# Kernel optimization log

Hardware: AMD Instinct MI355X
Metric: run time of the kernel (lower is better)

The kernel has to match this reference:

```python
import jax, jax.numpy as jnp
import numpy as np

EMBED = 1280
H = 20
D = 64
MAX_CACHE_LEN = 2048
NEG = -1e30


def setup_inputs() -> dict:
    key = jax.random.key(0)
    ks = jax.random.split(key, 6)
    w = lambda k: jax.random.normal(k, (EMBED, EMBED), dtype=jnp.float32) * 0.02
    return {
        "hidden_states": jax.random.normal(ks[0], (1, 2048, EMBED), dtype=jnp.float32),
        "wq": w(ks[1]), "bq": jnp.zeros((EMBED,), jnp.float32),
        "wk": w(ks[2]),
        "wv": w(ks[3]), "bv": jnp.zeros((EMBED,), jnp.float32),
        "wo": w(ks[4]), "bo": jnp.zeros((EMBED,), jnp.float32),
        "pos_int": 0,
    }


def reference(hidden_states, wq, bq, wk, wv, bv, wo, bo, pos_int):
    B, T, E = hidden_states.shape
    scale = D ** -0.5
    # projections (torch Linear: x @ W^T + b); Whisper k_proj has no bias
    q = (hidden_states @ wq.T + bq).reshape(B, T, H, D).transpose(0, 2, 1, 3)
    k = (hidden_states @ wk.T).reshape(B, T, H, D).transpose(0, 2, 1, 3)
    v = (hidden_states @ wv.T + bv).reshape(B, T, H, D).transpose(0, 2, 1, 3)
    # static KV-cache update (ETKVCache.update): write k,v at [pos:pos+T]
    k_cache = jnp.zeros((B, H, MAX_CACHE_LEN, D), hidden_states.dtype)
    v_cache = jnp.zeros((B, H, MAX_CACHE_LEN, D), hidden_states.dtype)
    k_cache = jax.lax.dynamic_update_slice(k_cache, k, (0, 0, pos_int, 0))
    v_cache = jax.lax.dynamic_update_slice(v_cache, v, (0, 0, pos_int, 0))
    end_pos = pos_int + T
    k_win = k_cache[:, :, :end_pos, :]  # [B,H,S,D]
    v_win = v_cache[:, :, :end_pos, :]
    # SDPA with is_causal=True: torch uses top-left aligned tril(T, S) mask
    scores = jnp.einsum("bhtd,bhsd->bhts", q, k_win) * scale
    mask = jnp.tril(jnp.ones((T, end_pos), dtype=bool))
    scores = jnp.where(mask, scores, NEG)
    attn = jax.nn.softmax(scores, axis=-1)
    out = jnp.einsum("bhts,bhsd->bhtd", attn, v_win)
    out = out.transpose(0, 2, 1, 3).reshape(B, T, H * D)
    return out @ wo.T + bo
```

## Files before the change

kernel.cpp:

```cpp
#include <hip/hip_runtime.h>
#include <hip/hip_bf16.h>

typedef __bf16 bf16;
typedef __bf16 bf16x8 __attribute__((ext_vector_type(8)));
typedef float  f32x4  __attribute__((ext_vector_type(4)));
typedef float  f32x16 __attribute__((ext_vector_type(16)));
typedef unsigned int u32;
typedef u32 u32x4 __attribute__((ext_vector_type(4)));

#define AS1 __attribute__((address_space(1)))
#define AS3 __attribute__((address_space(3)))

#define T_LEN 2048
#define EMB   1280
#define NH    20
#define HD    64

#define NCHUNK_PER_HEAD 40

#define QSCALE 0.18033688011112042f

__device__ __forceinline__ void gl_lds16(const void* gsrc, void* ldst) {
  __builtin_amdgcn_global_load_lds((AS1 void*)const_cast<void*>(gsrc),
                                   (AS3 void*)ldst, 16, 0, 0);
}

__global__ __launch_bounds__(256) void cvt_all(
    const float* __restrict__ hs, const float* __restrict__ wq,
    const float* __restrict__ wk, const float* __restrict__ wv,
    const float* __restrict__ wo, bf16* __restrict__ out) {
  const int HS8 = T_LEN * EMB / 8;
  const int W8  = EMB * EMB / 8;
  int i = blockIdx.x * 256 + threadIdx.x;
  const float* src;
  bf16* dst;
  int off;
  if (i < HS8)              { src = hs; dst = out;                              off = i; }
  else if (i < HS8 + W8)    { src = wq; dst = out + (size_t)T_LEN * EMB;        off = i - HS8; }
  else if (i < HS8 + 2*W8)  { src = wk; dst = out + (size_t)T_LEN*EMB +   (size_t)EMB*EMB; off = i - HS8 - W8; }
  else if (i < HS8 + 3*W8)  { src = wv; dst = out + (size_t)T_LEN*EMB + 2*(size_t)EMB*EMB; off = i - HS8 - 2*W8; }
  else if (i < HS8 + 4*W8)  { src = wo; dst = out + (size_t)T_LEN*EMB + 3*(size_t)EMB*EMB; off = i - HS8 - 3*W8; }
  else return;
  const float4* p4 = (const float4*)src;
  float4 a = p4[2 * off], b = p4[2 * off + 1];
  bf16x8 o;
  o[0] = (bf16)a.x; o[1] = (bf16)a.y; o[2] = (bf16)a.z; o[3] = (bf16)a.w;
  o[4] = (bf16)b.x; o[5] = (bf16)b.y; o[6] = (bf16)b.z; o[7] = (bf16)b.w;
  *(bf16x8*)(dst + (size_t)off * 8) = o;
}

template<int MT>
__global__ __launch_bounds__(256, 2) void gemm_nt(
    const bf16* __restrict__ hsb, const bf16* __restrict__ aob,
    const bf16* __restrict__ wqb, const bf16* __restrict__ wkb,
    const bf16* __restrict__ wvb, const bf16* __restrict__ wob,
    const float* __restrict__ bq, const float* __restrict__ bv,
    const float* __restrict__ bo,
    bf16* __restrict__ Qb, bf16* __restrict__ Kb, bf16* __restrict__ VTb,
    float* __restrict__ Out, int kind)
{
  constexpr int BM = MT * 32;
  constexpr int NK = EMB / 64;
  __shared__ alignas(16) bf16 As[2][BM * 64];
  __shared__ alignas(16) bf16 Bs[2][128 * 64];

  const int mode = (kind == 0) ? (int)blockIdx.y : 3;
  const bf16* A = (kind == 0) ? hsb : aob;
  const bf16* B = (mode == 0) ? wqb : (mode == 1) ? wkb : (mode == 2) ? wvb : wob;

  const int bm = blockIdx.x / 10;
  const int bn = blockIdx.x % 10;
  const int lane = threadIdx.x & 63;
  const int w = threadIdx.x >> 6;
  const int wr = w >> 1, wc = w & 1;
  const int g = lane >> 4, c = lane & 15;

  const f32x4 z4 = {0.f, 0.f, 0.f, 0.f};
  f32x4 acc[MT][4];
  #pragma unroll
  for (int i = 0; i < MT; ++i)
    #pragma unroll
    for (int j = 0; j < 4; ++j) acc[i][j] = z4;

  auto STAGE = [&](int b, int kt) {
    #pragma unroll
    for (int i = 0; i < MT; ++i) {
      const int call = w * MT + i;
      const int slot = call * 1024 + lane * 16;
      const int row = slot >> 7;
      const int scb = (slot & 127) ^ ((row & 7) << 4);
      gl_lds16((const char*)A + (size_t)(bm * BM + row) * (EMB * 2) + kt * 128 + scb,
               (char*)As[b] + call * 1024);
    }
    #pragma unroll
    for (int i = 0; i < 4; ++i) {
      const int call = w * 4 + i;
      const int slot = call * 1024 + lane * 16;
      const int row = slot >> 7;
      const int scb = (slot & 127) ^ ((row & 7) << 4);
      gl_lds16((const char*)B + (size_t)(bn * 128 + row) * (EMB * 2) + kt * 128 + scb,
               (char*)Bs[b] + call * 1024);
    }
  };

  STAGE(0, 0);
  for (int kt = 0; kt < NK; ++kt) {
    const int cur = kt & 1;
    STAGE(cur ^ 1, kt + 1 < NK ? kt + 1 : kt);
    if constexpr (MT == 4) asm volatile("s_waitcnt vmcnt(8)" ::: "memory");
    else                   asm volatile("s_waitcnt vmcnt(6)" ::: "memory");
    __builtin_amdgcn_s_barrier();
    asm volatile("" ::: "memory");
    const bf16* Asc = As[cur];
    const bf16* Bsc = Bs[cur];
    #pragma unroll
    for (int kc = 0; kc < 2; ++kc) {
      bf16x8 af[MT], bfr[4];
      #pragma unroll
      for (int mt = 0; mt < MT; ++mt) {
        const int row = wr * (MT * 16) + mt * 16 + c;
        const int off = row * 128 + ((kc * 64 + g * 16) ^ ((row & 7) << 4));
        af[mt] = *(const bf16x8*)((const char*)Asc + off);
      }
      #pragma unroll
      for (int nt = 0; nt < 4; ++nt) {
        const int row = wc * 64 + nt * 16 + c;
        const int off = row * 128 + ((kc * 64 + g * 16) ^ ((row & 7) << 4));
        bfr[nt] = *(const bf16x8*)((const char*)Bsc + off);
      }
      #pragma unroll
      for (int mt = 0; mt < MT; ++mt)
        #pragma unroll
        for (int nt = 0; nt < 4; ++nt)
          acc[mt][nt] = __builtin_amdgcn_mfma_f32_16x16x32_bf16(af[mt], bfr[nt],
                                                                acc[mt][nt], 0, 0, 0);
    }
    asm volatile("" ::: "memory");
    __builtin_amdgcn_s_barrier();
  }

  #pragma unroll
  for (int mt = 0; mt < MT; ++mt) {
    const int t0 = bm * BM + wr * (MT * 16) + mt * 16 + g * 4;
    #pragma unroll
    for (int nt = 0; nt < 4; ++nt) {
      const int n = bn * 128 + wc * 64 + nt * 16 + c;
      const int h = n >> 6, d = n & 63;
      #pragma unroll
      for (int r = 0; r < 4; ++r) {
        const int t = t0 + r;
        float v = acc[mt][nt][r];
        if (mode == 0) {
          v = (v + bq[n]) * QSCALE;
          Qb[((size_t)h * T_LEN + t) * HD + d] = (bf16)v;
        } else if (mode == 1) {
          Kb[((size_t)h * T_LEN + t) * HD + d] = (bf16)v;
        } else if (mode == 2) {
          v += bv[n];
          VTb[((size_t)h * HD + d) * T_LEN + t] = (bf16)v;
        } else {
          Out[(size_t)t * EMB + n] = v + bo[n];
        }
      }
    }
  }
}

__global__ __launch_bounds__(256, 4) void attn_fwd(
    const bf16* __restrict__ Qb, const bf16* __restrict__ Kb,
    const bf16* __restrict__ VTb, bf16* __restrict__ AOb,
    bf16* __restrict__ Pob, float* __restrict__ Pml)
{
  __shared__ alignas(16) bf16 kbuf[2][64 * 64];
  __shared__ alignas(16) bf16 vbuf[2][64 * 64];

  const int bid = blockIdx.x;
  const int h   = bid / NCHUNK_PER_HEAD;
  const int idx = (NCHUNK_PER_HEAD - 1) - bid % NCHUNK_PER_HEAD;
  int qb, ch, nch;
  if (idx < 4)       { qb = idx;                ch = 0;      nch = 1; }
  else if (idx < 12) { int t = idx - 4;  qb = 4 + (t >> 1);  ch = t & 1;  nch = 2; }
  else if (idx < 24) { int t = idx - 12; qb = 8 + t / 3;     ch = t % 3;  nch = 3; }
  else               { int t = idx - 24; qb = 12 + (t >> 2); ch = t & 3;  nch = 4; }
  const int nj = 2 * qb + 2;
  const int j0 = ch * 8;
  const int j1 = (j0 + 8 < nj) ? j0 + 8 : nj;

  const int lane = threadIdx.x & 63;
  const int w  = threadIdx.x >> 6;
  const int l31 = lane & 31;
  const int hi  = lane >> 5;
  const int q0 = qb * 128;
  const int q  = q0 + w * 32 + l31;

  bf16x8 qf[4];
  {
    const char* qrow = (const char*)Qb + ((size_t)h * T_LEN + q) * (HD * 2);
    #pragma unroll
    for (int ds = 0; ds < 4; ++ds)
      qf[ds] = *(const bf16x8*)(qrow + ds * 32 + hi * 16);
  }

  f32x16 oacc[2];
  #pragma unroll
  for (int r = 0; r < 16; ++r) { oacc[0][r] = 0.f; oacc[1][r] = 0.f; }
  float m_r = -1e30f, ls = 0.f;

  auto STAGE = [&](int b, int j) {
    const int s0 = j * 64;
    #pragma unroll
    for (int i = 0; i < 2; ++i) {
      const int call = w * 2 + i;
      const int slot = call * 1024 + lane * 16;
      const int row = slot >> 7;
      const int col = (slot & 127) ^ ((row & 7) << 4);
      gl_lds16((const char*)Kb + ((size_t)h * T_LEN + s0 + row) * (HD * 2) + col,
               (char*)kbuf[b] + call * 1024);
      gl_lds16((const char*)VTb + (((size_t)h * HD + row) * T_LEN + s0) * 2 + col,
               (char*)vbuf[b] + call * 1024);
    }
  };

  auto AFRAG = [&](const bf16* buf, int rblk, int colb) -> bf16x8 {
    const int row = rblk * 32 + l31;
    const int off = row * 128 + ((colb + hi * 16) ^ ((row & 7) << 4));
    return *(const bf16x8*)((const char*)buf + off);
  };

  STAGE(0, j0);
  int cur = 0;
  for (int j = j0; j < j1; ++j) {
    STAGE(cur ^ 1, j + 1 < j1 ? j + 1 : j);
    asm volatile("s_waitcnt vmcnt(4)" ::: "memory");
    __builtin_amdgcn_s_barrier();
    asm volatile("" ::: "memory");

    f32x16 sv[2];
    #pragma unroll
    for (int r = 0; r < 16; ++r) { sv[0][r] = 0.f; sv[1][r] = 0.f; }
    #pragma unroll
    for (int ds = 0; ds < 4; ++ds) {
      #pragma unroll
      for (int sb = 0; sb < 2; ++sb) {
        bf16x8 kf = AFRAG(kbuf[cur], sb, ds * 32);
        sv[sb] = __builtin_amdgcn_mfma_f32_32x32x16_bf16(kf, qf[ds], sv[sb], 0, 0, 0);
      }
    }

    if (j >= 2 * qb) {
      const int s0 = j * 64;
      #pragma unroll
      for (int sb = 0; sb < 2; ++sb)
        #pragma unroll
        for (int r = 0; r < 16; ++r) {
          const int s = s0 + sb * 32 + (r & 3) + 8 * (r >> 2) + 4 * hi;
          if (s > q) sv[sb][r] = -1e30f;
        }
    }

    float pm = sv[0][0];
    #pragma unroll
    for (int r = 1; r < 16; ++r) pm = fmaxf(pm, sv[0][r]);
    #pragma unroll
    for (int r = 0; r < 16; ++r) pm = fmaxf(pm, sv[1][r]);
    pm = fmaxf(pm, __shfl_xor(pm, 32));
    const float mn = fmaxf(m_r, pm);
    const float sc = __builtin_amdgcn_exp2f(m_r - mn);
    m_r = mn;
    float ps = 0.f;
    #pragma unroll
    for (int sb = 0; sb < 2; ++sb)
      #pragma unroll
      for (int r = 0; r < 16; ++r) {
        const float p = __builtin_amdgcn_exp2f(sv[sb][r] - mn);
        sv[sb][r] = p;
        ps += p;
      }
    ls = ls * sc + ps;
    oacc[0] *= sc;
    oacc[1] *= sc;

    u32 wds[16], xds[16];
    #pragma unroll
    for (int i = 0; i < 8; ++i) {
      asm("v_cvt_pk_bf16_f32 %0, %1, %2" : "=v"(wds[i])     : "v"(sv[0][2*i]), "v"(sv[0][2*i+1]));
      asm("v_cvt_pk_bf16_f32 %0, %1, %2" : "=v"(wds[8 + i]) : "v"(sv[1][2*i]), "v"(sv[1][2*i+1]));
    }
    #pragma unroll
    for (int i = 0; i < 16; ++i) xds[i] = (u32)__shfl_xor((int)wds[i], 32);

    #pragma unroll
    for (int ks = 0; ks < 4; ++ks) {
      const int o = (ks >> 1) * 8 + (ks & 1) * 4;
      u32x4 fw;
      fw.x = hi ? xds[o + 2] : wds[o];
      fw.y = hi ? xds[o + 3] : wds[o + 1];
      fw.z = hi ? wds[o + 2] : xds[o];
      fw.w = hi ? wds[o + 3] : xds[o + 1];
      bf16x8 pf = __builtin_bit_cast(bf16x8, fw);
      #pragma unroll
      for (int db = 0; db < 2; ++db) {
        bf16x8 vf = AFRAG(vbuf[cur], db, ks * 32);
        oacc[db] = __builtin_amdgcn_mfma_f32_32x32x16_bf16(vf, pf, oacc[db], 0, 0, 0);
      }
    }

    asm volatile("" ::: "memory");
    __builtin_amdgcn_s_barrier();
    cur ^= 1;
  }

  const float lt = ls + __shfl_xor(ls, 32);

  if (nch == 1) {
    const float inv = 1.f / lt;
    char* orow = (char*)AOb + ((size_t)q * EMB + h * HD) * 2;
    #pragma unroll
    for (int db = 0; db < 2; ++db)
      #pragma unroll
      for (int i = 0; i < 8; ++i) {
        const float lo = oacc[db][2 * i] * inv;
        const float hv = oacc[db][2 * i + 1] * inv;
        u32 pk;
        asm("v_cvt_pk_bf16_f32 %0, %1, %2" : "=v"(pk) : "v"(lo), "v"(hv));
        const int d = db * 32 + 8 * (i >> 1) + 2 * (i & 1) + 4 * hi;
        *(u32*)(orow + d * 2) = pk;
      }
  } else {
    const int pi = h * NCHUNK_PER_HEAD + idx;
    const int rowloc = w * 32 + l31;
    bf16* pr = Pob + ((size_t)pi * 128 + rowloc) * 64;
    #pragma unroll
    for (int db = 0; db < 2; ++db)
      #pragma unroll
      for (int i = 0; i < 8; ++i) {
        u32 pk;
        asm("v_cvt_pk_bf16_f32 %0, %1, %2" : "=v"(pk) : "v"(oacc[db][2*i]), "v"(oacc[db][2*i+1]));
        const int d = db * 32 + 8 * (i >> 1) + 2 * (i & 1) + 4 * hi;
        *(u32*)((char*)pr + d * 2) = pk;
      }
    if (hi == 0) {
      float* ml = Pml + ((size_t)pi * 128 + rowloc) * 2;
      ml[0] = m_r;
      ml[1] = lt;
    }
  }
}

__global__ __launch_bounds__(256) void attn_combine(
    const bf16* __restrict__ Pob, const float* __restrict__ Pml,
    bf16* __restrict__ AOb)
{
  const int gw = (blockIdx.x * 256 + threadIdx.x) >> 6;
  const int lane = threadIdx.x & 63;
  const int h  = gw / 1536;
  const int rr = gw % 1536;
  const int qb = 4 + rr / 128;
  const int rl = rr % 128;
  const int nch   = (qb < 8) ? 2 : (qb < 12) ? 3 : 4;
  const int ibase = (qb < 8) ? 4 + 2 * (qb - 4)
                   : (qb < 12) ? 12 + 3 * (qb - 8)
                   : 24 + 4 * (qb - 12);
  const int pi0 = h * NCHUNK_PER_HEAD + ibase;

  float mv[4], lv[4];
  float m = -1e30f;
  for (int c2 = 0; c2 < nch; ++c2) {
    const float* ml = Pml + ((size_t)(pi0 + c2) * 128 + rl) * 2;
    mv[c2] = ml[0];
    lv[c2] = ml[1];
    m = fmaxf(m, mv[c2]);
  }
  float acc = 0.f, l = 0.f;
  for (int c2 = 0; c2 < nch; ++c2) {
    const float sc = __builtin_amdgcn_exp2f(mv[c2] - m);
    const float ov = (float)Pob[((size_t)(pi0 + c2) * 128 + rl) * 64 + lane];
    acc += sc * ov;
    l   += sc * lv[c2];
  }
  const int qrow = qb * 128 + rl;
  AOb[(size_t)qrow * EMB + h * HD + lane] = (bf16)(acc / l);
}

extern "C" void kernel_launch(void* const* d_in, const int* in_sizes, int n_in,
                              void* d_out, int out_size, void* d_ws, size_t ws_size,
                              hipStream_t stream) {
  const float* hs = (const float*)d_in[0];
  const float* wq = (const float*)d_in[1];
  const float* bq = (const float*)d_in[2];
  const float* wk = (const float*)d_in[3];
  const float* wv = (const float*)d_in[4];
  const float* bv = (const float*)d_in[5];
  const float* wo = (const float*)d_in[6];
  const float* bo = (const float*)d_in[7];

  bf16* p = (bf16*)d_ws;
  bf16* hsb = p;  p += (size_t)T_LEN * EMB;
  bf16* wqb = p;  p += (size_t)EMB * EMB;
  bf16* wkb = p;  p += (size_t)EMB * EMB;
  bf16* wvb = p;  p += (size_t)EMB * EMB;
  bf16* wob = p;  p += (size_t)EMB * EMB;
  bf16* Qb  = p;  p += (size_t)NH * T_LEN * HD;
  bf16* Kb  = p;  p += (size_t)NH * T_LEN * HD;
  bf16* VTb = p;  p += (size_t)NH * HD * T_LEN;
  bf16* AOb = p;  p += (size_t)T_LEN * EMB;

  bf16*  Pob = (bf16*)d_ws;
  float* Pml = (float*)((char*)d_ws + (size_t)NH * NCHUNK_PER_HEAD * 128 * 64 * 2);

  const int TOT8 = T_LEN * EMB / 8 + 4 * (EMB * EMB / 8);
  cvt_all<<<(TOT8 + 255) / 256, 256, 0, stream>>>(hs, wq, wk, wv, wo, (bf16*)d_ws);

  gemm_nt<4><<<dim3(160, 3), 256, 0, stream>>>(hsb, AOb, wqb, wkb, wvb, wob, bq, bv, bo,
                                               Qb, Kb, VTb, (float*)d_out, 0);
  attn_fwd<<<dim3(NH * NCHUNK_PER_HEAD), 256, 0, stream>>>(Qb, Kb, VTb, AOb, Pob, Pml);
  attn_combine<<<dim3(NH * 1536 / 4), 256, 0, stream>>>(Pob, Pml, AOb);
  gemm_nt<2><<<dim3(320, 1), 256, 0, stream>>>(hsb, AOb, wqb, wkb, wvb, wob, bq, bv, bo,
                                               Qb, Kb, VTb, (float*)d_out, 1);
}
```

Before: 119.5 us.

## Enlarge GEMM block tiles and reorder block indices for weight reuse

The GEMM kernel is re-parameterised by warp rows. The QKV projection now uses 512-thread blocks with 256x128 tiles over a flat 240-block grid, and the output projection uses 128x128 tiles over 160 blocks. Block indices are remapped so consecutive blocks share the same weight column tile across row tiles, aiming for better L2 reuse of B and less redundant global traffic per FLOP. In exchange, both grids now launch fewer blocks than there are CUs, and the larger LDS footprint limits occupancy to one block per CU for the QKV GEMM.

```diff
diff --git a/kernel.cpp b/kernel.cpp
--- a/kernel.cpp
+++ b/kernel.cpp
@@ -49,8 +49,8 @@
   *(bf16x8*)(dst + (size_t)off * 8) = o;
 }
 
-template<int MT>
-__global__ __launch_bounds__(256, 2) void gemm_nt(
+template<int WR>
+__global__ __launch_bounds__(WR * 128, 2) void gemm_nt(
     const bf16* __restrict__ hsb, const bf16* __restrict__ aob,
     const bf16* __restrict__ wqb, const bf16* __restrict__ wkb,
     const bf16* __restrict__ wvb, const bf16* __restrict__ wob,
@@ -59,45 +59,55 @@
     bf16* __restrict__ Qb, bf16* __restrict__ Kb, bf16* __restrict__ VTb,
     float* __restrict__ Out, int kind)
 {
-  constexpr int BM = MT * 32;
+  constexpr int BM = WR * 64;
+  constexpr int NW = WR * 2;
+  constexpr int CH_B = 16 / NW;
   constexpr int NK = EMB / 64;
   __shared__ alignas(16) bf16 As[2][BM * 64];
   __shared__ alignas(16) bf16 Bs[2][128 * 64];
 
-  const int mode = (kind == 0) ? (int)blockIdx.y : 3;
-  const bf16* A = (kind == 0) ? hsb : aob;
+  int bm, bn, mode;
+  const bf16* A;
+  if (kind == 0) {
+    const int g = blockIdx.x % 24, i = blockIdx.x / 24;
+    bm = g & 7; mode = g >> 3; bn = i;
+    A = hsb;
+  } else {
+    const int g = blockIdx.x % 16, i = blockIdx.x / 16;
+    bm = g; mode = 3; bn = i;
+    A = aob;
+  }
   const bf16* B = (mode == 0) ? wqb : (mode == 1) ? wkb : (mode == 2) ? wvb : wob;
-
-  const int bm = blockIdx.x / 10;
-  const int bn = blockIdx.x % 10;
+  const int rowbase = bm * BM;
+
   const int lane = threadIdx.x & 63;
   const int w = threadIdx.x >> 6;
   const int wr = w >> 1, wc = w & 1;
-  const int g = lane >> 4, c = lane & 15;
+  const int g4 = lane >> 4, c = lane & 15;
 
   const f32x4 z4 = {0.f, 0.f, 0.f, 0.f};
-  f32x4 acc[MT][4];
+  f32x4 acc[4][4];
   #pragma unroll
-  for (int i = 0; i < MT; ++i)
+  for (int i = 0; i < 4; ++i)
     #pragma unroll
     for (int j = 0; j < 4; ++j) acc[i][j] = z4;
 
   auto STAGE = [&](int b, int kt) {
-    #pragma unroll
-    for (int i = 0; i < MT; ++i) {
-      const int call = w * MT + i;
-      const int slot = call * 1024 + lane * 16;
-      const int row = slot >> 7;
-      const int scb = (slot & 127) ^ ((row & 7) << 4);
-      gl_lds16((const char*)A + (size_t)(bm * BM + row) * (EMB * 2) + kt * 128 + scb,
-               (char*)As[b] + call * 1024);
-    }
     #pragma unroll
     for (int i = 0; i < 4; ++i) {
       const int call = w * 4 + i;
       const int slot = call * 1024 + lane * 16;
       const int row = slot >> 7;
       const int scb = (slot & 127) ^ ((row & 7) << 4);
+      gl_lds16((const char*)A + (size_t)(rowbase + row) * (EMB * 2) + kt * 128 + scb,
+               (char*)As[b] + call * 1024);
+    }
+    #pragma unroll
+    for (int i = 0; i < CH_B; ++i) {
+      const int call = w * CH_B + i;
+      const int slot = call * 1024 + lane * 16;
+      const int row = slot >> 7;
+      const int scb = (slot & 127) ^ ((row & 7) << 4);
       gl_lds16((const char*)B + (size_t)(bn * 128 + row) * (EMB * 2) + kt * 128 + scb,
                (char*)Bs[b] + call * 1024);
     }
@@ -107,29 +117,29 @@
   for (int kt = 0; kt < NK; ++kt) {
     const int cur = kt & 1;
     STAGE(cur ^ 1, kt + 1 < NK ? kt + 1 : kt);
-    if constexpr (MT == 4) asm volatile("s_waitcnt vmcnt(8)" ::: "memory");
-    else                   asm volatile("s_waitcnt vmcnt(6)" ::: "memory");
+    if constexpr (WR == 4) asm volatile("s_waitcnt vmcnt(6)" ::: "memory");
+    else                   asm volatile("s_waitcnt vmcnt(8)" ::: "memory");
     __builtin_amdgcn_s_barrier();
     asm volatile("" ::: "memory");
     const bf16* Asc = As[cur];
     const bf16* Bsc = Bs[cur];
     #pragma unroll
     for (int kc = 0; kc < 2; ++kc) {
-      bf16x8 af[MT], bfr[4];
-      #pragma unroll
-      for (int mt = 0; mt < MT; ++mt) {
-        const int row = wr * (MT * 16) + mt * 16 + c;
-        const int off = row * 128 + ((kc * 64 + g * 16) ^ ((row & 7) << 4));
+      bf16x8 af[4], bfr[4];
+      #pragma unroll
+      for (int mt = 0; mt < 4; ++mt) {
+        const int row = wr * 64 + mt * 16 + c;
+        const int off = row * 128 + ((kc * 64 + g4 * 16) ^ ((row & 7) << 4));
         af[mt] = *(const bf16x8*)((const char*)Asc + off);
       }
       #pragma unroll
       for (int nt = 0; nt < 4; ++nt) {
         const int row = wc * 64 + nt * 16 + c;
-        const int off = row * 128 + ((kc * 64 + g * 16) ^ ((row & 7) << 4));
+        const int off = row * 128 + ((kc * 64 + g4 * 16) ^ ((row & 7) << 4));
         bfr[nt] = *(const bf16x8*)((const char*)Bsc + off);
       }
       #pragma unroll
-      for (int mt = 0; mt < MT; ++mt)
+      for (int mt = 0; mt < 4; ++mt)
         #pragma unroll
         for (int nt = 0; nt < 4; ++nt)
           acc[mt][nt] = __builtin_amdgcn_mfma_f32_16x16x32_bf16(af[mt], bfr[nt],
@@ -140,8 +150,8 @@
   }
 
   #pragma unroll
-  for (int mt = 0; mt < MT; ++mt) {
-    const int t0 = bm * BM + wr * (MT * 16) + mt * 16 + g * 4;
+  for (int mt = 0; mt < 4; ++mt) {
+    const int t0 = rowbase + wr * 64 + mt * 16 + g4 * 4;
     #pragma unroll
     for (int nt = 0; nt < 4; ++nt) {
       const int n = bn * 128 + wc * 64 + nt * 16 + c;
@@ -411,10 +421,10 @@
   const int TOT8 = T_LEN * EMB / 8 + 4 * (EMB * EMB / 8);
   cvt_all<<<(TOT8 + 255) / 256, 256, 0, stream>>>(hs, wq, wk, wv, wo, (bf16*)d_ws);
 
-  gemm_nt<4><<<dim3(160, 3), 256, 0, stream>>>(hsb, AOb, wqb, wkb, wvb, wob, bq, bv, bo,
-                                               Qb, Kb, VTb, (float*)d_out, 0);
+  gemm_nt<4><<<dim3(240), 512, 0, stream>>>(hsb, AOb, wqb, wkb, wvb, wob, bq, bv, bo,
+                                            Qb, Kb, VTb, (float*)d_out, 0);
   attn_fwd<<<dim3(NH * NCHUNK_PER_HEAD), 256, 0, stream>>>(Qb, Kb, VTb, AOb, Pob, Pml);
   attn_combine<<<dim3(NH * 1536 / 4), 256, 0, stream>>>(Pob, Pml, AOb);
-  gemm_nt<2><<<dim3(320, 1), 256, 0, stream>>>(hsb, AOb, wqb, wkb, wvb, wob, bq, bv, bo,
-                                               Qb, Kb, VTb, (float*)d_out, 1);
-}
+  gemm_nt<2><<<dim3(160), 256, 0, stream>>>(hsb, AOb, wqb, wkb, wvb, wob, bq, bv, bo,
+                                            Qb, Kb, VTb, (float*)d_out, 1);
+}
```

After: 136.2 us. 14.0% more time.
